# Optimization experiments

Measured on AMD Instinct MI355X. Metric: run time of the kernel, lower is better.

## Reference

```python
import jax, jax.numpy as jnp
import numpy as np
import math

B, SEQ, E, H, NB, NHYP = 4, 1024, 512, 8, 64, 6
V, HID, NC, ENC = 32000, 2048, 6, 6
DH = E // H


def _pos_encoding(n, e, dtype):
    pos = jnp.arange(n, dtype=dtype)[:, None]
    div = jnp.exp(-jnp.arange(0, e, 2, dtype=dtype) * (math.log(10000.0) / e))
    ang = pos * div  # [n, e/2]
    pe = jnp.zeros((n, e), dtype)
    pe = pe.at[:, 0::2].set(jnp.sin(ang))
    pe = pe.at[:, 1::2].set(jnp.cos(ang))
    return pe


def _layer_norm(x, g, b):
    m = x.mean(-1, keepdims=True)
    v = ((x - m) ** 2).mean(-1, keepdims=True)
    return (x - m) / jnp.sqrt(v + 1e-5) * g + b


def _lsh_attention(x, Wq, bq, Wv, bv, hyper):
    b, n, e = x.shape
    q = x @ Wq + bq
    v = x @ Wv + bv
    q4 = q.reshape(b, n, H, DH)  # [b,n,h,d]
    v4 = v.reshape(b, n, H, DH)
    # bucket hashing: append bias 1, project on hyperplanes, binarize, binary-encode
    aug = jnp.concatenate([q4, jnp.ones((b, n, H, 1), q.dtype)], axis=-1)
    proj = jnp.einsum('bnhe,ey->bnhy', aug, hyper)
    bits = (proj >= 0).astype(q.dtype)
    pows = (2 ** jnp.arange(NHYP)).astype(q.dtype)
    buckets = jnp.einsum('bnhy,y->bnh', bits, pows).astype(jnp.int32)
    bh = buckets.transpose(0, 2, 1)  # [b,h,n]
    qh = q4.transpose(0, 2, 1, 3)  # [b,h,n,d]
    vh = v4.transpose(0, 2, 1, 3)
    scores = jnp.einsum('bhnd,bhmd->bhnm', qh, qh) / math.sqrt(e)
    # torch code zeroes q rows at their OWN bucket and sums q_c @ q_c^T over all
    # NB buckets; that equals scores * (NB - 2 + [bucket_i == bucket_j]) exactly.
    same = bh[:, :, :, None] == bh[:, :, None, :]
    count = (NB - 2 + same.astype(jnp.int32)).astype(scores.dtype)
    attn = jax.nn.softmax(scores * count, axis=-1)
    out = jnp.einsum('bhnm,bhmd->bhnd', attn, vh)
    return out.transpose(0, 2, 1, 3).reshape(b, n, e)


def setup_inputs() -> dict:
    key = jax.random.key(0)
    ks = jax.random.split(key, 16)
    s = 0.02
    emb = jax.random.normal(ks[0], (V, E), jnp.float32) * s
    emb = emb.at[V - 1].set(0.0)  # padding_idx row
    return dict(
        inputs=jax.random.randint(ks[1], (B, SEQ), 0, V),
        emb=emb,
        gamma=jnp.ones((E,), jnp.float32),
        beta=jnp.zeros((E,), jnp.float32),
        Wq=jax.random.normal(ks[2], (E, E), jnp.float32) * s,
        bq=jnp.zeros((E,), jnp.float32),
        Wv=jax.random.normal(ks[3], (E, E), jnp.float32) * s,
        bv=jnp.zeros((E,), jnp.float32),
        hyper=jax.random.normal(ks[4], (DH + 1, NHYP), jnp.float32),
        W1=jax.random.normal(ks[5], (E, HID), jnp.float32) * s,
        b1=jnp.zeros((HID,), jnp.float32),
        W2=jax.random.normal(ks[6], (HID, E), jnp.float32) * s,
        b2=jnp.zeros((E,), jnp.float32),
        Wm=jax.random.normal(ks[7], (E * SEQ, NC), jnp.float32) * 0.002,
        bm=jnp.zeros((NC,), jnp.float32),
    )


def reference(inputs, emb, gamma, beta, Wq, bq, Wv, bv, hyper, W1, b1, W2, b2, Wm, bm):
    x = emb[inputs]  # [B, SEQ, E]
    x = x + _pos_encoding(x.shape[1], x.shape[2], x.dtype)
    for _ in range(ENC):  # shared weights across encoders
        a = _lsh_attention(x, Wq, bq, Wv, bv, hyper)
        x = _layer_norm(a, gamma, beta)
        x = jax.nn.relu(x @ W1 + b1) @ W2 + b2 + x
        x = _layer_norm(x, gamma, beta)
    x = x.reshape(x.shape[0], -1)
    return x @ Wm + bm  # [B, NC]
```

## Files before the change

kernel.cpp:

```cpp
#include <hip/hip_runtime.h>
#include <hip/hip_bf16.h>
#include <math.h>

#define B_    4
#define SEQ_  1024
#define E_    512
#define H_    8
#define DH_   64
#define NHYP_ 6
#define HID_  2048
#define NC_   6
#define ENC_  6
#define BH_   (B_*H_)
#define NCAT_ 1088

typedef __attribute__((ext_vector_type(8))) short short8;
typedef __attribute__((ext_vector_type(4))) float f32x4;

static __device__ __forceinline__ float wave_rsum(float v){
#pragma unroll
  for(int o=32;o;o>>=1) v += __shfl_down(v,o,64);
  return v;
}
static __device__ __forceinline__ ushort f2b(float v){
  __hip_bfloat16 h = __float2bfloat16(v);
  return *(ushort*)&h;
}
static __device__ __forceinline__ float b2f(ushort u){
  unsigned int x = ((unsigned int)u) << 16;
  return *(float*)&x;
}
static __device__ __forceinline__ void gload16(const void* g, void* l){
  __builtin_amdgcn_global_load_lds(
      (const __attribute__((address_space(1))) void*)g,
      (__attribute__((address_space(3))) void*)l,
      16, 0, 0);
}

__global__ void embed_pe_kernel(const int* __restrict__ inp, const float* __restrict__ emb,
                                float* __restrict__ x, ushort* __restrict__ xh){
  int row = blockIdx.x;
  int s = row & (SEQ_-1);
  int idx = inp[row];
  const float* er = emb + (size_t)idx*E_;
  float* xr = x + (size_t)row*E_;
  ushort* hr = xh + (size_t)row*E_;
  for(int c=threadIdx.x;c<E_;c+=blockDim.x){
    int i = c>>1;
    float div = expf(-(float)i * 0.0359778920780319646f);
    float ang = (float)s * div;
    float pe = (c&1) ? cosf(ang) : sinf(ang);
    float v = er[c] + pe;
    xr[c] = v;
    hr[c] = f2b(v);
  }
}

__global__ __launch_bounds__(256) void transpose_cast(
    const float* __restrict__ W, ushort* __restrict__ Wt, int K, int N){
  __shared__ float T[32][33];
  int tx = threadIdx.x & 31, ty = threadIdx.x >> 5;
  int n0 = blockIdx.x*32, k0 = blockIdx.y*32;
#pragma unroll
  for(int i=0;i<32;i+=8) T[ty+i][tx] = W[(size_t)(k0+ty+i)*N + n0+tx];
  __syncthreads();
#pragma unroll
  for(int i=0;i<32;i+=8)
    Wt[(size_t)(n0+ty+i)*K + k0+tx] = f2b(T[tx][ty+i]);
}

__global__ void wproj_build(const float* __restrict__ Wq, const float* __restrict__ hyper,
                            ushort* __restrict__ WcatT){
  int t = blockIdx.x*256 + threadIdx.x;
  int c = t >> 9, k = t & 511;
  float s = 0.f;
  if(c < 48){
    int h = c/6, y = c%6;
    const float* wr = Wq + (size_t)k*E_ + h*DH_;
    for(int d=0;d<DH_;++d) s += wr[d]*hyper[d*NHYP_+y];
  }
  WcatT[(size_t)(1024+c)*E_ + k] = f2b(s);
}

__global__ void bias_build(const float* __restrict__ bq, const float* __restrict__ bv,
                           const float* __restrict__ hyper, float* __restrict__ bcat){
  int t = blockIdx.x*256 + threadIdx.x;
  if(t >= NCAT_) return;
  float v;
  if(t < 512) v = bq[t];
  else if(t < 1024) v = bv[t-512];
  else if(t < 1072){
    int c = t - 1024, h = c/6, y = c%6;
    float s = hyper[DH_*NHYP_ + y];
    for(int d=0;d<DH_;++d) s += bq[h*DH_+d]*hyper[d*NHYP_+y];
    v = s;
  } else v = 0.f;
  bcat[t] = v;
}

template<int BM, int BN, int EPI>
__global__ __launch_bounds__(256) void gemm_mfma(
    const ushort* __restrict__ A, const ushort* __restrict__ Bt,
    const float* __restrict__ bias, const float* __restrict__ res,
    void* __restrict__ C0, void* __restrict__ C1, void* __restrict__ C2,
    int M, int N, int K)
{
  constexpr int MI = BM/32, NI = BN/32;
  constexpr int ACH = BM/32, BCH = BN/32;
  __shared__ ushort As[2][BM*64];
  __shared__ ushort Bs[2][BN*64];
  int tid = threadIdx.x;
  int w = tid>>6, lane = tid&63, g = lane>>4, li = lane&15;
  int wr = w>>1, wc = w&1;
  int bm = blockIdx.y*BM, bn = blockIdx.x*BN;
  int NK = K>>6;

  f32x4 acc[MI][NI] = {};

  auto issue = [&](int ks, int pb){
    int k0 = ks*64;
#pragma unroll
    for(int it=0; it<ACH; ++it){
      int c = it*256 + tid; int r = c>>3; int kq = ((c&7)^(r&7))*8;
      gload16(&A[(size_t)(bm+r)*K + k0 + kq], &As[pb][it*2048 + w*512]);
    }
#pragma unroll
    for(int it=0; it<BCH; ++it){
      int c = it*256 + tid; int r = c>>3; int kq = ((c&7)^(r&7))*8;
      gload16(&Bt[(size_t)(bn+r)*K + k0 + kq], &Bs[pb][it*2048 + w*512]);
    }
  };

  issue(0, 0);
  __syncthreads();
  for(int ks=0; ks<NK; ++ks){
    if(ks+1 < NK) issue(ks+1, (ks+1)&1);
    int pb = ks&1;
#pragma unroll
    for(int kc=0; kc<2; ++kc){
      short8 af[MI], bf[NI];
#pragma unroll
      for(int mi=0;mi<MI;++mi)
        af[mi] = *(const short8*)&As[pb][(wr*(BM/2)+mi*16+li)*64 + (((kc*4+g)^(li&7))*8)];
#pragma unroll
      for(int ni=0;ni<NI;++ni)
        bf[ni] = *(const short8*)&Bs[pb][(wc*(BN/2)+ni*16+li)*64 + (((kc*4+g)^(li&7))*8)];
#pragma unroll
      for(int mi=0;mi<MI;++mi)
#pragma unroll
        for(int ni=0;ni<NI;++ni)
          acc[mi][ni] = __builtin_amdgcn_mfma_f32_16x16x32_bf16(af[mi], bf[ni], acc[mi][ni], 0,0,0);
    }
    __syncthreads();
  }

#pragma unroll
  for(int mi=0;mi<MI;++mi){
    int rbase = bm + wr*(BM/2) + mi*16 + g*4;
#pragma unroll
    for(int ni=0;ni<NI;++ni){
      int cc = bn + wc*(BN/2) + ni*16 + li;
      float bv = bias[cc];
      float vv[4];
#pragma unroll
      for(int j=0;j<4;++j) vv[j] = acc[mi][ni][j] + bv;
      if(EPI==0){
#pragma unroll
        for(int j=0;j<4;++j) ((float*)C0)[(size_t)(rbase+j)*N + cc] = vv[j];
      } else if(EPI==1){
#pragma unroll
        for(int j=0;j<4;++j) ((ushort*)C0)[(size_t)(rbase+j)*N + cc] = f2b(fmaxf(vv[j],0.0f));
      } else if(EPI==2){
#pragma unroll
        for(int j=0;j<4;++j){
          size_t o = (size_t)(rbase+j)*N + cc;
          ((float*)C0)[o] = vv[j] + res[o];
        }
      } else {
        if(cc < 512){
          int h = cc>>6, d = cc&63;
#pragma unroll
          for(int j=0;j<4;++j){
            int r = rbase + j;
            int b = r>>10, n = r&1023;
            ((ushort*)C1)[(((size_t)(b*8+h))*1024 + n)*64 + d] = f2b(vv[j]);
          }
        } else if(cc < 1024){
          int cl = cc - 512; int h = cl>>6, d = cl&63;
          int b = rbase>>10, n = rbase&1023;
          ushort4 pk;
          pk.x = f2b(vv[0]); pk.y = f2b(vv[1]); pk.z = f2b(vv[2]); pk.w = f2b(vv[3]);
          *(ushort4*)&((ushort*)C2)[(((size_t)(b*8+h))*64 + d)*1024 + n] = pk;
        } else if(cc < 1072){
#pragma unroll
          for(int j=0;j<4;++j)
            ((float*)C0)[(size_t)(rbase+j)*64 + (cc-1024)] = vv[j];
        }
      }
    }
  }
}

__global__ __launch_bounds__(256) void encode_kernel(
    const ushort* __restrict__ Qh, const float* __restrict__ Pr,
    int* __restrict__ buckets, float* __restrict__ qn2){
  int t = blockIdx.x*256 + threadIdx.x;
  int h = t & 7, row = t >> 3;
  int b = row >> 10, n = row & 1023;
  int bhn = (b*8+h)*1024 + n;
  const short8* qp = (const short8*)&Qh[(size_t)bhn*DH_];
  float s2 = 0.f;
#pragma unroll
  for(int c=0;c<8;++c){
    short8 v = qp[c];
#pragma unroll
    for(int j=0;j<8;++j){
      float f = b2f((ushort)v[j]);
      s2 += f*f;
    }
  }
  qn2[bhn] = s2;
  const float* pr = Pr + (size_t)row*64 + h*NHYP_;
  int bk = 0;
#pragma unroll
  for(int y=0;y<NHYP_;++y) bk |= (pr[y] >= 0.0f) ? (1<<y) : 0;
  buckets[bhn] = bk;
}

__global__ __launch_bounds__(256) void attn_mfma_kernel(
    const ushort* __restrict__ Qh,
    const ushort* __restrict__ Vt,
    const int* __restrict__ buckets,
    const float* __restrict__ qn2,
    float* __restrict__ outp)
{
  int bid = blockIdx.x;
  int bh = bid & 31;
  int qt = bid >> 5;
  int b = bh >> 3, h = bh & 7;
  int tid = threadIdx.x;
  int w = tid >> 6, lane = tid & 63;
  int g = lane >> 4, li = lane & 15;

  __shared__ ushort Ks[2][64*64];
  __shared__ ushort Vs[2][64*64];
  __shared__ ushort Ps[64*68];
  __shared__ int bks[2][64];
  __shared__ int bqs[64];
  __shared__ float mred[4];

  const ushort* Qbase = Qh + (size_t)bh*SEQ_*DH_;
  const ushort* Vbase = Vt + (size_t)bh*DH_*SEQ_;
  const int* Bb = buckets + bh*SEQ_;
  const float* qn = qn2 + bh*SEQ_;
  int q0 = qt*64;

  auto issue = [&](int kt, int pb){
    int j0 = kt*64;
#pragma unroll
    for(int it=0; it<2; ++it){
      int c = it*256 + tid; int r = c>>3; int ks = ((c&7)^(r&7))*8;
      gload16(&Qbase[(size_t)(j0+r)*DH_ + ks], &Ks[pb][it*2048 + w*512]);
      gload16(&Vbase[(size_t)r*SEQ_ + j0 + ks], &Vs[pb][it*2048 + w*512]);
    }
    if(tid < 16) gload16(&Bb[j0 + tid*4], &bks[pb][0]);
  };

  issue(0, 0);
  short8 qa[2];
  int qrow = q0 + w*16 + li;
#pragma unroll
  for(int kc=0; kc<2; ++kc)
    qa[kc] = *(const short8*)&Qbase[(size_t)qrow*DH_ + kc*32 + g*8];
  if(tid < 64) bqs[tid] = Bb[q0 + tid];

  float mx = 0.f;
  for(int i=tid;i<SEQ_;i+=256) mx = fmaxf(mx, qn[i]);
#pragma unroll
  for(int o=32;o;o>>=1) mx = fmaxf(mx, __shfl_xor(mx, o, 64));
  if(lane==0) mred[w] = mx;
  __syncthreads();
  float maxn = sqrtf(fmaxf(fmaxf(mred[0],mred[1]), fmaxf(mred[2],mred[3])));

  const float invsq = 0.04419417382415922f;
  const float c63 = invsq * 63.0f;
  float Mrow[4];
#pragma unroll
  for(int i=0;i<4;++i)
    Mrow[i] = c63 * sqrtf(qn[q0 + w*16 + g*4 + i]) * maxn + 1.0f;

  f32x4 acc_o[4] = {};
  float psum[4] = {0.f,0.f,0.f,0.f};

  for(int kt=0; kt<16; ++kt){
    if(kt < 15) issue(kt+1, (kt+1)&1);
    int pb = kt&1;

    f32x4 accs[4];
    __builtin_amdgcn_s_setprio(1);
#pragma unroll
    for(int nt=0; nt<4; ++nt){
      f32x4 z = {};
#pragma unroll
      for(int kc=0; kc<2; ++kc){
        short8 kb = *(const short8*)&Ks[pb][(nt*16+li)*64 + (((kc*4+g)^(li&7))*8)];
        z = __builtin_amdgcn_mfma_f32_16x16x32_bf16(qa[kc], kb, z, 0,0,0);
      }
      accs[nt] = z;
    }
    __builtin_amdgcn_s_setprio(0);
    int bkc[4];
#pragma unroll
    for(int nt=0;nt<4;++nt) bkc[nt] = bks[pb][nt*16 + li];

#pragma unroll
    for(int i=0;i<4;++i){
      int rloc = w*16 + g*4 + i;
      int bq = bqs[rloc];
      float rs = 0.f;
#pragma unroll
      for(int nt=0;nt<4;++nt){
        float cnt = (bkc[nt] == bq) ? 63.f : 62.f;
        float e = __expf(accs[nt][i] * (invsq * cnt) - Mrow[i]);
        rs += e;
        Ps[rloc*68 + nt*16 + li] = f2b(e);
      }
      psum[i] += rs;
    }
    __builtin_amdgcn_s_setprio(1);
#pragma unroll
    for(int dt=0; dt<4; ++dt){
      f32x4 z = acc_o[dt];
#pragma unroll
      for(int kc=0; kc<2; ++kc){
        short8 pa = *(const short8*)&Ps[(w*16+li)*68 + kc*32 + g*8];
        short8 vb = *(const short8*)&Vs[pb][(dt*16+li)*64 + (((kc*4+g)^(li&7))*8)];
        z = __builtin_amdgcn_mfma_f32_16x16x32_bf16(pa, vb, z, 0,0,0);
      }
      acc_o[dt] = z;
    }
    __builtin_amdgcn_s_setprio(0);
    __syncthreads();
  }
#pragma unroll
  for(int i=0;i<4;++i){
#pragma unroll
    for(int o=8;o;o>>=1) psum[i] += __shfl_xor(psum[i], o, 64);
  }
  float* obase = outp + ((size_t)(b*SEQ_ + q0 + w*16 + g*4))*E_ + h*DH_;
#pragma unroll
  for(int i=0;i<4;++i){
    float inv = 1.0f / fmaxf(psum[i], 1e-35f);
#pragma unroll
    for(int dt=0;dt<4;++dt)
      obase[(size_t)i*E_ + dt*16 + li] = acc_o[dt][i] * inv;
  }
}

__global__ __launch_bounds__(256) void ln_kernel(
    const float* __restrict__ in, const float* __restrict__ g,
    const float* __restrict__ bb, float* __restrict__ outp,
    ushort* __restrict__ oh){
  int row = blockIdx.x*4 + (threadIdx.x>>6);
  int lane = threadIdx.x & 63;
  const float4* xr = (const float4*)(in + (size_t)row*E_);
  float4 v0 = xr[lane*2], v1 = xr[lane*2+1];
  float s  = v0.x+v0.y+v0.z+v0.w + v1.x+v1.y+v1.z+v1.w;
  float s2 = v0.x*v0.x+v0.y*v0.y+v0.z*v0.z+v0.w*v0.w
           + v1.x*v1.x+v1.y*v1.y+v1.z*v1.z+v1.w*v1.w;
#pragma unroll
  for(int o=32;o;o>>=1){ s += __shfl_xor(s,o,64); s2 += __shfl_xor(s2,o,64); }
  float mean = s*(1.0f/E_);
  float var  = s2*(1.0f/E_) - mean*mean;
  float inv = rsqrtf(var + 1e-5f);
  const float4* g4 = (const float4*)(g) + lane*2;
  const float4* b4 = (const float4*)(bb) + lane*2;
  float4 g0 = g4[0], g1 = g4[1], b0 = b4[0], b1 = b4[1];
  float4 y0, y1;
  y0.x=(v0.x-mean)*inv*g0.x+b0.x; y0.y=(v0.y-mean)*inv*g0.y+b0.y;
  y0.z=(v0.z-mean)*inv*g0.z+b0.z; y0.w=(v0.w-mean)*inv*g0.w+b0.w;
  y1.x=(v1.x-mean)*inv*g1.x+b1.x; y1.y=(v1.y-mean)*inv*g1.y+b1.y;
  y1.z=(v1.z-mean)*inv*g1.z+b1.z; y1.w=(v1.w-mean)*inv*g1.w+b1.w;
  float4* orow = (float4*)(outp + (size_t)row*E_) + lane*2;
  orow[0] = y0; orow[1] = y1;
  ushort hs[8];
  hs[0]=f2b(y0.x); hs[1]=f2b(y0.y); hs[2]=f2b(y0.z); hs[3]=f2b(y0.w);
  hs[4]=f2b(y1.x); hs[5]=f2b(y1.y); hs[6]=f2b(y1.z); hs[7]=f2b(y1.w);
  *(uint4*)&oh[(size_t)row*E_ + lane*8] = *(uint4*)hs;
}

__global__ void final_partial(const float* __restrict__ x, const float* __restrict__ Wm,
                              float* __restrict__ part){
  int b  = blockIdx.x >> 7;
  int ch = blockIdx.x & 127;
  const float* xb = x + (size_t)b*SEQ_*E_;
  int k0 = ch*4096;
  float acc[NC_] = {};
  for(int k=k0+threadIdx.x; k<k0+4096; k+=256){
    float xv = xb[k];
    const float* wrow = Wm + (size_t)k*NC_;
#pragma unroll
    for(int c=0;c<NC_;++c) acc[c] += xv*wrow[c];
  }
#pragma unroll
  for(int c=0;c<NC_;++c) acc[c] = wave_rsum(acc[c]);
  __shared__ float r[4][NC_];
  int w = threadIdx.x>>6, lane = threadIdx.x&63;
  if(lane==0){
#pragma unroll
    for(int c=0;c<NC_;++c) r[w][c] = acc[c];
  }
  __syncthreads();
  if(threadIdx.x==0){
#pragma unroll
    for(int c=0;c<NC_;++c)
      part[(size_t)blockIdx.x*NC_ + c] = r[0][c]+r[1][c]+r[2][c]+r[3][c];
  }
}

__global__ void final_reduce(const float* __restrict__ part, const float* __restrict__ bm,
                             float* __restrict__ out){
  int t = threadIdx.x;
  if(t >= B_*NC_) return;
  int b = t / NC_, c = t % NC_;
  float s = bm[c];
  for(int i=0;i<128;++i) s += part[(size_t)(b*128+i)*NC_ + c];
  out[t] = s;
}

extern "C" void kernel_launch(void* const* d_in, const int* in_sizes, int n_in,
                              void* d_out, int out_size, void* d_ws, size_t ws_size,
                              hipStream_t stream){
  const int*   inp   = (const int*)d_in[0];
  const float* emb   = (const float*)d_in[1];
  const float* gamma = (const float*)d_in[2];
  const float* beta  = (const float*)d_in[3];
  const float* Wq    = (const float*)d_in[4];
  const float* bq    = (const float*)d_in[5];
  const float* Wv    = (const float*)d_in[6];
  const float* bv    = (const float*)d_in[7];
  const float* hyper = (const float*)d_in[8];
  const float* W1    = (const float*)d_in[9];
  const float* b1    = (const float*)d_in[10];
  const float* W2    = (const float*)d_in[11];
  const float* b2    = (const float*)d_in[12];
  const float* Wm    = (const float*)d_in[13];
  const float* bm    = (const float*)d_in[14];
  float* out = (float*)d_out;

  char* ws = (char*)d_ws;
  size_t off = 0;
  auto alloc = [&](size_t bytes)->void*{
    void* p = ws + off; off += (bytes + 255) & ~(size_t)255; return p;
  };
  const size_t NTOK = (size_t)B_*SEQ_;
  float*  X    = (float*)alloc(NTOK*E_*sizeof(float));
  float*  A    = (float*)alloc(NTOK*E_*sizeof(float));
  float*  Pr   = (float*)alloc(NTOK*64*sizeof(float));
  ushort* Xh   = (ushort*)alloc(NTOK*E_*sizeof(ushort));
  ushort* Hh   = (ushort*)alloc(NTOK*HID_*sizeof(ushort));
  int*    Bk   = (int*)  alloc((size_t)BH_*SEQ_*sizeof(int));
  float*  Qn2  = (float*)alloc((size_t)BH_*SEQ_*sizeof(float));
  float*  Pp   = (float*)alloc((size_t)B_*128*NC_*sizeof(float));
  ushort* Qh   = (ushort*)alloc((size_t)BH_*SEQ_*DH_*sizeof(ushort));
  ushort* Vt   = (ushort*)alloc((size_t)BH_*DH_*SEQ_*sizeof(ushort));
  ushort* WcatT= (ushort*)alloc((size_t)NCAT_*E_*sizeof(ushort));
  ushort* W1T  = (ushort*)alloc((size_t)HID_*E_*sizeof(ushort));
  ushort* W2T  = (ushort*)alloc((size_t)E_*HID_*sizeof(ushort));
  float*  bcat = (float*)alloc(NCAT_*sizeof(float));
  (void)ws_size; (void)in_sizes; (void)n_in; (void)out_size;

  transpose_cast<<<dim3(E_/32,  E_/32),  256, 0, stream>>>(Wq, WcatT, E_, E_);
  transpose_cast<<<dim3(E_/32,  E_/32),  256, 0, stream>>>(Wv, WcatT + (size_t)512*E_, E_, E_);
  wproj_build<<<128, 256, 0, stream>>>(Wq, hyper, WcatT);
  transpose_cast<<<dim3(HID_/32,E_/32),  256, 0, stream>>>(W1, W1T, E_, HID_);
  transpose_cast<<<dim3(E_/32,  HID_/32),256, 0, stream>>>(W2, W2T, HID_, E_);
  bias_build<<<5, 256, 0, stream>>>(bq, bv, hyper, bcat);

  embed_pe_kernel<<<B_*SEQ_, 256, 0, stream>>>(inp, emb, X, Xh);

  dim3 gQV(NCAT_/64, (B_*SEQ_)/128);
  dim3 gF1(HID_/128, (B_*SEQ_)/128);
  dim3 gF2(E_/64,    (B_*SEQ_)/128);
  for(int l=0;l<ENC_;++l){
    gemm_mfma<128,64,5><<<gQV, 256, 0, stream>>>(Xh, WcatT, bcat, nullptr, Pr, Qh, Vt, B_*SEQ_, NCAT_, E_);
    encode_kernel<<<(B_*SEQ_*H_)/256, 256, 0, stream>>>(Qh, Pr, Bk, Qn2);
    attn_mfma_kernel<<<BH_*16, 256, 0, stream>>>(Qh, Vt, Bk, Qn2, A);
    ln_kernel<<<B_*SEQ_/4, 256, 0, stream>>>(A, gamma, beta, X, Xh);
    gemm_mfma<128,128,1><<<gF1, 256, 0, stream>>>(Xh, W1T, b1, nullptr, Hh, nullptr, nullptr, B_*SEQ_, HID_, E_);
    gemm_mfma<128,64,2><<<gF2, 256, 0, stream>>>(Hh, W2T, b2, X, A, nullptr, nullptr, B_*SEQ_, E_, HID_);
    ln_kernel<<<B_*SEQ_/4, 256, 0, stream>>>(A, gamma, beta, X, Xh);
  }
  final_partial<<<B_*128, 256, 0, stream>>>(X, Wm, Pp);
  final_reduce<<<1, 32, 0, stream>>>(Pp, bm, out);
}
```

Measured before the change: 650.5 us.

## Split attention keys across two blocks and fuse partial combine into layernorm

Attention now splits the key range into two halves, each handled by a separate block. Each block writes unnormalized partial outputs and row sums, and a new combine_ln kernel adds the halves, normalizes and applies layernorm. This doubles the attention grid from 512 to 1024 blocks to fill the GPU's CUs better, and the QV and FF2 GEMMs move to 64-row tiles for more blocks. It works because the softmax uses a fixed per-row bound rather than a running max, so the halves can be summed directly. The cost is extra partial-output traffic (two fp32 copies of the attention output) plus a per-block duplicated max-norm scan.

```diff
diff --git a/kernel.cpp b/kernel.cpp
--- a/kernel.cpp
+++ b/kernel.cpp
@@ -12,6 +12,7 @@
 #define NC_   6
 #define ENC_  6
 #define BH_   (B_*H_)
+#define NTOK_ 4096
 #define NCAT_ 1088
 
 typedef __attribute__((ext_vector_type(8))) short short8;
@@ -232,11 +233,13 @@
     const ushort* __restrict__ Vt,
     const int* __restrict__ buckets,
     const float* __restrict__ qn2,
-    float* __restrict__ outp)
+    float* __restrict__ Op,
+    float* __restrict__ Sp)
 {
   int bid = blockIdx.x;
-  int bh = bid & 31;
-  int qt = bid >> 5;
+  int bh   = bid & 31;
+  int half = (bid >> 5) & 1;
+  int qt   = bid >> 6;
   int b = bh >> 3, h = bh & 7;
   int tid = threadIdx.x;
   int w = tid >> 6, lane = tid & 63;
@@ -254,6 +257,7 @@
   const int* Bb = buckets + bh*SEQ_;
   const float* qn = qn2 + bh*SEQ_;
   int q0 = qt*64;
+  int kt0 = half*8;
 
   auto issue = [&](int kt, int pb){
     int j0 = kt*64;
@@ -266,7 +270,7 @@
     if(tid < 16) gload16(&Bb[j0 + tid*4], &bks[pb][0]);
   };
 
-  issue(0, 0);
+  issue(kt0, 0);
   short8 qa[2];
   int qrow = q0 + w*16 + li;
 #pragma unroll
@@ -292,9 +296,10 @@
   f32x4 acc_o[4] = {};
   float psum[4] = {0.f,0.f,0.f,0.f};
 
-  for(int kt=0; kt<16; ++kt){
-    if(kt < 15) issue(kt+1, (kt+1)&1);
-    int pb = kt&1;
+  for(int t=0; t<8; ++t){
+    int kt = kt0 + t;
+    if(t < 7) issue(kt+1, (t+1)&1);
+    int pb = t&1;
 
     f32x4 accs[4];
     __builtin_amdgcn_s_setprio(1);
@@ -347,14 +352,59 @@
 #pragma unroll
     for(int o=8;o;o>>=1) psum[i] += __shfl_xor(psum[i], o, 64);
   }
-  float* obase = outp + ((size_t)(b*SEQ_ + q0 + w*16 + g*4))*E_ + h*DH_;
+  float* obase = Op + (size_t)half*NTOK_*E_
+               + ((size_t)(b*SEQ_ + q0 + w*16 + g*4))*E_ + h*DH_;
 #pragma unroll
   for(int i=0;i<4;++i){
-    float inv = 1.0f / fmaxf(psum[i], 1e-35f);
 #pragma unroll
     for(int dt=0;dt<4;++dt)
-      obase[(size_t)i*E_ + dt*16 + li] = acc_o[dt][i] * inv;
-  }
+      obase[(size_t)i*E_ + dt*16 + li] = acc_o[dt][i];
+  }
+  if(li == 0){
+    float* sp = Sp + (size_t)half*BH_*SEQ_ + (size_t)bh*SEQ_ + q0 + w*16 + g*4;
+#pragma unroll
+    for(int i=0;i<4;++i) sp[i] = psum[i];
+  }
+}
+
+__global__ __launch_bounds__(256) void combine_ln(
+    const float* __restrict__ Op, const float* __restrict__ Sp,
+    const float* __restrict__ g, const float* __restrict__ bb,
+    float* __restrict__ outp, ushort* __restrict__ oh){
+  int row = blockIdx.x*4 + (threadIdx.x>>6);
+  int lane = threadIdx.x & 63;
+  int b = row >> 10, n = row & 1023;
+  int h = lane >> 3;
+  size_t sidx = (size_t)(b*8+h)*SEQ_ + n;
+  float ps = Sp[sidx] + Sp[(size_t)BH_*SEQ_ + sidx];
+  float inv0 = 1.0f / fmaxf(ps, 1e-35f);
+  const float4* o1 = (const float4*)(Op + (size_t)row*E_) + lane*2;
+  const float4* o2 = (const float4*)(Op + (size_t)NTOK_*E_ + (size_t)row*E_) + lane*2;
+  float4 v0 = o1[0], v1 = o1[1], u0 = o2[0], u1 = o2[1];
+  v0.x=(v0.x+u0.x)*inv0; v0.y=(v0.y+u0.y)*inv0; v0.z=(v0.z+u0.z)*inv0; v0.w=(v0.w+u0.w)*inv0;
+  v1.x=(v1.x+u1.x)*inv0; v1.y=(v1.y+u1.y)*inv0; v1.z=(v1.z+u1.z)*inv0; v1.w=(v1.w+u1.w)*inv0;
+  float s  = v0.x+v0.y+v0.z+v0.w + v1.x+v1.y+v1.z+v1.w;
+  float s2 = v0.x*v0.x+v0.y*v0.y+v0.z*v0.z+v0.w*v0.w
+           + v1.x*v1.x+v1.y*v1.y+v1.z*v1.z+v1.w*v1.w;
+#pragma unroll
+  for(int o=32;o;o>>=1){ s += __shfl_xor(s,o,64); s2 += __shfl_xor(s2,o,64); }
+  float mean = s*(1.0f/E_);
+  float var  = s2*(1.0f/E_) - mean*mean;
+  float inv = rsqrtf(var + 1e-5f);
+  const float4* g4 = (const float4*)(g) + lane*2;
+  const float4* b4 = (const float4*)(bb) + lane*2;
+  float4 g0 = g4[0], g1 = g4[1], b0 = b4[0], b1 = b4[1];
+  float4 y0, y1;
+  y0.x=(v0.x-mean)*inv*g0.x+b0.x; y0.y=(v0.y-mean)*inv*g0.y+b0.y;
+  y0.z=(v0.z-mean)*inv*g0.z+b0.z; y0.w=(v0.w-mean)*inv*g0.w+b0.w;
+  y1.x=(v1.x-mean)*inv*g1.x+b1.x; y1.y=(v1.y-mean)*inv*g1.y+b1.y;
+  y1.z=(v1.z-mean)*inv*g1.z+b1.z; y1.w=(v1.w-mean)*inv*g1.w+b1.w;
+  float4* orow = (float4*)(outp + (size_t)row*E_) + lane*2;
+  orow[0] = y0; orow[1] = y1;
+  ushort hs[8];
+  hs[0]=f2b(y0.x); hs[1]=f2b(y0.y); hs[2]=f2b(y0.z); hs[3]=f2b(y0.w);
+  hs[4]=f2b(y1.x); hs[5]=f2b(y1.y); hs[6]=f2b(y1.z); hs[7]=f2b(y1.w);
+  *(uint4*)&oh[(size_t)row*E_ + lane*8] = *(uint4*)hs;
 }
 
 __global__ __launch_bounds__(256) void ln_kernel(
@@ -457,6 +507,8 @@
   float*  X    = (float*)alloc(NTOK*E_*sizeof(float));
   float*  A    = (float*)alloc(NTOK*E_*sizeof(float));
   float*  Pr   = (float*)alloc(NTOK*64*sizeof(float));
+  float*  Op   = (float*)alloc((size_t)2*NTOK*E_*sizeof(float));
+  float*  Sp   = (float*)alloc((size_t)2*BH_*SEQ_*sizeof(float));
   ushort* Xh   = (ushort*)alloc(NTOK*E_*sizeof(ushort));
   ushort* Hh   = (ushort*)alloc(NTOK*HID_*sizeof(ushort));
   int*    Bk   = (int*)  alloc((size_t)BH_*SEQ_*sizeof(int));
@@ -479,16 +531,16 @@
 
   embed_pe_kernel<<<B_*SEQ_, 256, 0, stream>>>(inp, emb, X, Xh);
 
-  dim3 gQV(NCAT_/64, (B_*SEQ_)/128);
+  dim3 gQV(NCAT_/64, (B_*SEQ_)/64);
   dim3 gF1(HID_/128, (B_*SEQ_)/128);
-  dim3 gF2(E_/64,    (B_*SEQ_)/128);
+  dim3 gF2(E_/64,    (B_*SEQ_)/64);
   for(int l=0;l<ENC_;++l){
-    gemm_mfma<128,64,5><<<gQV, 256, 0, stream>>>(Xh, WcatT, bcat, nullptr, Pr, Qh, Vt, B_*SEQ_, NCAT_, E_);
+    gemm_mfma<64,64,5><<<gQV, 256, 0, stream>>>(Xh, WcatT, bcat, nullptr, Pr, Qh, Vt, B_*SEQ_, NCAT_, E_);
     encode_kernel<<<(B_*SEQ_*H_)/256, 256, 0, stream>>>(Qh, Pr, Bk, Qn2);
-    attn_mfma_kernel<<<BH_*16, 256, 0, stream>>>(Qh, Vt, Bk, Qn2, A);
-    ln_kernel<<<B_*SEQ_/4, 256, 0, stream>>>(A, gamma, beta, X, Xh);
+    attn_mfma_kernel<<<BH_*32, 256, 0, stream>>>(Qh, Vt, Bk, Qn2, Op, Sp);
+    combine_ln<<<B_*SEQ_/4, 256, 0, stream>>>(Op, Sp, gamma, beta, X, Xh);
     gemm_mfma<128,128,1><<<gF1, 256, 0, stream>>>(Xh, W1T, b1, nullptr, Hh, nullptr, nullptr, B_*SEQ_, HID_, E_);
-    gemm_mfma<128,64,2><<<gF2, 256, 0, stream>>>(Hh, W2T, b2, X, A, nullptr, nullptr, B_*SEQ_, E_, HID_);
+    gemm_mfma<64,64,2><<<gF2, 256, 0, stream>>>(Hh, W2T, b2, X, A, nullptr, nullptr, B_*SEQ_, E_, HID_);
     ln_kernel<<<B_*SEQ_/4, 256, 0, stream>>>(A, gamma, beta, X, Xh);
   }
   final_partial<<<B_*128, 256, 0, stream>>>(X, Wm, Pp);
```

New measurement: 642.4 us. Within noise of the previous version (-1.2%).

## Fuse bucket encoding into QV GEMM epilogue and split-K the FFN down-projection

Applied to the files above, without the earlier changes.

The QV projection GEMM epilogue now computes the squared query norms and the hash bucket ids directly, with a cross-lane reduction and shared-memory staging, so the separate encode kernel and the fp32 projection buffer go away. Its tile shrinks to 64x64 for more blocks. The W2 GEMM uses a 2-way split-K with 64x64 tiles and writes two partial results. A new ln2 kernel sums the partials, bias and residual before the layer norm. This trades one launch and some traffic for extra partial-buffer reads and writes and added shared memory in every GEMM instantiation.

```diff
diff --git a/kernel.cpp b/kernel.cpp
--- a/kernel.cpp
+++ b/kernel.cpp
@@ -12,6 +12,7 @@
 #define NC_   6
 #define ENC_  6
 #define BH_   (B_*H_)
+#define NTOK_ 4096
 #define NCAT_ 1088
 
 typedef __attribute__((ext_vector_type(8))) short short8;
@@ -103,22 +104,26 @@
     const ushort* __restrict__ A, const ushort* __restrict__ Bt,
     const float* __restrict__ bias, const float* __restrict__ res,
     void* __restrict__ C0, void* __restrict__ C1, void* __restrict__ C2,
-    int M, int N, int K)
+    void* __restrict__ C3, int M, int N, int K)
 {
   constexpr int MI = BM/32, NI = BN/32;
   constexpr int ACH = BM/32, BCH = BN/32;
   __shared__ ushort As[2][BM*64];
   __shared__ ushort Bs[2][BN*64];
+  __shared__ float epi[64*49];
   int tid = threadIdx.x;
   int w = tid>>6, lane = tid&63, g = lane>>4, li = lane&15;
   int wr = w>>1, wc = w&1;
   int bm = blockIdx.y*BM, bn = blockIdx.x*BN;
-  int NK = K>>6;
+  int kz = blockIdx.z;
+  int kcnt = K / (int)gridDim.z;
+  int kbase = kz * kcnt;
+  int NK = kcnt >> 6;
 
   f32x4 acc[MI][NI] = {};
 
   auto issue = [&](int ks, int pb){
-    int k0 = ks*64;
+    int k0 = kbase + ks*64;
 #pragma unroll
     for(int it=0; it<ACH; ++it){
       int c = it*256 + tid; int r = c>>3; int kq = ((c&7)^(r&7))*8;
@@ -154,22 +159,108 @@
     __syncthreads();
   }
 
+  if(EPI==5){
+    if(bn < 512){
+      int h = bn >> 6;
+#pragma unroll
+      for(int mi=0;mi<MI;++mi){
+        int rbase = bm + wr*(BM/2) + mi*16 + g*4;
+        float q2s[4] = {0.f,0.f,0.f,0.f};
+#pragma unroll
+        for(int ni=0;ni<NI;++ni){
+          int cc = bn + wc*(BN/2) + ni*16 + li;
+          float bv = bias[cc];
+          int d = cc & 63;
+#pragma unroll
+          for(int j=0;j<4;++j){
+            float vvf = acc[mi][ni][j] + bv;
+            ushort ub = f2b(vvf);
+            int r = rbase + j; int b = r>>10, n = r&1023;
+            ((ushort*)C1)[(((size_t)(b*8+h))*1024 + n)*64 + d] = ub;
+            float f = b2f(ub);
+            q2s[j] += f*f;
+          }
+        }
+#pragma unroll
+        for(int j=0;j<4;++j){
+#pragma unroll
+          for(int o=8;o;o>>=1) q2s[j] += __shfl_xor(q2s[j], o, 64);
+        }
+        if(li==0){
+#pragma unroll
+          for(int j=0;j<4;++j)
+            epi[(wr*(BM/2)+mi*16+g*4+j)*2 + wc] = q2s[j];
+        }
+      }
+      __syncthreads();
+      if(tid < 64){
+        int r = bm + tid; int b = r>>10, n = r&1023;
+        ((float*)C3)[((size_t)(b*8+h))*1024 + n] = epi[tid*2] + epi[tid*2+1];
+      }
+    } else if(bn < 1024){
+#pragma unroll
+      for(int mi=0;mi<MI;++mi){
+        int rbase = bm + wr*(BM/2) + mi*16 + g*4;
+        int b = rbase>>10, n = rbase&1023;
+#pragma unroll
+        for(int ni=0;ni<NI;++ni){
+          int cc = bn + wc*(BN/2) + ni*16 + li;
+          float bv = bias[cc];
+          int cl = cc - 512; int h = cl>>6, d = cl&63;
+          ushort4 pk;
+          pk.x = f2b(acc[mi][ni][0]+bv); pk.y = f2b(acc[mi][ni][1]+bv);
+          pk.z = f2b(acc[mi][ni][2]+bv); pk.w = f2b(acc[mi][ni][3]+bv);
+          *(ushort4*)&((ushort*)C2)[(((size_t)(b*8+h))*64 + d)*1024 + n] = pk;
+        }
+      }
+    } else {
+#pragma unroll
+      for(int mi=0;mi<MI;++mi){
+        int rloc = wr*(BM/2) + mi*16 + g*4;
+#pragma unroll
+        for(int ni=0;ni<NI;++ni){
+          int c = wc*(BN/2) + ni*16 + li;
+          if(c < 48){
+            float bv = bias[1024 + c];
+#pragma unroll
+            for(int j=0;j<4;++j)
+              epi[(rloc+j)*49 + c] = acc[mi][ni][j] + bv;
+          }
+        }
+      }
+      __syncthreads();
+      if(tid < 64){
+        int r = bm + tid; int b = r>>10, n = r&1023;
+#pragma unroll
+        for(int h=0;h<8;++h){
+          int bk = 0;
+#pragma unroll
+          for(int y=0;y<NHYP_;++y)
+            bk |= (epi[tid*49 + h*NHYP_ + y] >= 0.0f) ? (1<<y) : 0;
+          ((int*)C0)[((size_t)(b*8+h))*1024 + n] = bk;
+        }
+      }
+    }
+    return;
+  }
+
 #pragma unroll
   for(int mi=0;mi<MI;++mi){
     int rbase = bm + wr*(BM/2) + mi*16 + g*4;
 #pragma unroll
     for(int ni=0;ni<NI;++ni){
       int cc = bn + wc*(BN/2) + ni*16 + li;
-      float bv = bias[cc];
+      float bv = (EPI==6) ? 0.0f : bias[cc];
       float vv[4];
 #pragma unroll
       for(int j=0;j<4;++j) vv[j] = acc[mi][ni][j] + bv;
-      if(EPI==0){
-#pragma unroll
-        for(int j=0;j<4;++j) ((float*)C0)[(size_t)(rbase+j)*N + cc] = vv[j];
-      } else if(EPI==1){
+      if(EPI==1){
 #pragma unroll
         for(int j=0;j<4;++j) ((ushort*)C0)[(size_t)(rbase+j)*N + cc] = f2b(fmaxf(vv[j],0.0f));
+      } else if(EPI==6){
+        float* dst = (float*)C0 + (size_t)kz*M*N;
+#pragma unroll
+        for(int j=0;j<4;++j) dst[(size_t)(rbase+j)*N + cc] = vv[j];
       } else if(EPI==2){
 #pragma unroll
         for(int j=0;j<4;++j){
@@ -177,54 +268,11 @@
           ((float*)C0)[o] = vv[j] + res[o];
         }
       } else {
-        if(cc < 512){
-          int h = cc>>6, d = cc&63;
-#pragma unroll
-          for(int j=0;j<4;++j){
-            int r = rbase + j;
-            int b = r>>10, n = r&1023;
-            ((ushort*)C1)[(((size_t)(b*8+h))*1024 + n)*64 + d] = f2b(vv[j]);
-          }
-        } else if(cc < 1024){
-          int cl = cc - 512; int h = cl>>6, d = cl&63;
-          int b = rbase>>10, n = rbase&1023;
-          ushort4 pk;
-          pk.x = f2b(vv[0]); pk.y = f2b(vv[1]); pk.z = f2b(vv[2]); pk.w = f2b(vv[3]);
-          *(ushort4*)&((ushort*)C2)[(((size_t)(b*8+h))*64 + d)*1024 + n] = pk;
-        } else if(cc < 1072){
-#pragma unroll
-          for(int j=0;j<4;++j)
-            ((float*)C0)[(size_t)(rbase+j)*64 + (cc-1024)] = vv[j];
-        }
-      }
-    }
-  }
-}
-
-__global__ __launch_bounds__(256) void encode_kernel(
-    const ushort* __restrict__ Qh, const float* __restrict__ Pr,
-    int* __restrict__ buckets, float* __restrict__ qn2){
-  int t = blockIdx.x*256 + threadIdx.x;
-  int h = t & 7, row = t >> 3;
-  int b = row >> 10, n = row & 1023;
-  int bhn = (b*8+h)*1024 + n;
-  const short8* qp = (const short8*)&Qh[(size_t)bhn*DH_];
-  float s2 = 0.f;
-#pragma unroll
-  for(int c=0;c<8;++c){
-    short8 v = qp[c];
-#pragma unroll
-    for(int j=0;j<8;++j){
-      float f = b2f((ushort)v[j]);
-      s2 += f*f;
-    }
-  }
-  qn2[bhn] = s2;
-  const float* pr = Pr + (size_t)row*64 + h*NHYP_;
-  int bk = 0;
-#pragma unroll
-  for(int y=0;y<NHYP_;++y) bk |= (pr[y] >= 0.0f) ? (1<<y) : 0;
-  buckets[bhn] = bk;
+#pragma unroll
+        for(int j=0;j<4;++j) ((float*)C0)[(size_t)(rbase+j)*N + cc] = vv[j];
+      }
+    }
+  }
 }
 
 __global__ __launch_bounds__(256) void attn_mfma_kernel(
@@ -365,6 +413,47 @@
   int lane = threadIdx.x & 63;
   const float4* xr = (const float4*)(in + (size_t)row*E_);
   float4 v0 = xr[lane*2], v1 = xr[lane*2+1];
+  float s  = v0.x+v0.y+v0.z+v0.w + v1.x+v1.y+v1.z+v1.w;
+  float s2 = v0.x*v0.x+v0.y*v0.y+v0.z*v0.z+v0.w*v0.w
+           + v1.x*v1.x+v1.y*v1.y+v1.z*v1.z+v1.w*v1.w;
+#pragma unroll
+  for(int o=32;o;o>>=1){ s += __shfl_xor(s,o,64); s2 += __shfl_xor(s2,o,64); }
+  float mean = s*(1.0f/E_);
+  float var  = s2*(1.0f/E_) - mean*mean;
+  float inv = rsqrtf(var + 1e-5f);
+  const float4* g4 = (const float4*)(g) + lane*2;
+  const float4* b4 = (const float4*)(bb) + lane*2;
+  float4 g0 = g4[0], g1 = g4[1], b0 = b4[0], b1 = b4[1];
+  float4 y0, y1;
+  y0.x=(v0.x-mean)*inv*g0.x+b0.x; y0.y=(v0.y-mean)*inv*g0.y+b0.y;
+  y0.z=(v0.z-mean)*inv*g0.z+b0.z; y0.w=(v0.w-mean)*inv*g0.w+b0.w;
+  y1.x=(v1.x-mean)*inv*g1.x+b1.x; y1.y=(v1.y-mean)*inv*g1.y+b1.y;
+  y1.z=(v1.z-mean)*inv*g1.z+b1.z; y1.w=(v1.w-mean)*inv*g1.w+b1.w;
+  float4* orow = (float4*)(outp + (size_t)row*E_) + lane*2;
+  orow[0] = y0; orow[1] = y1;
+  ushort hs[8];
+  hs[0]=f2b(y0.x); hs[1]=f2b(y0.y); hs[2]=f2b(y0.z); hs[3]=f2b(y0.w);
+  hs[4]=f2b(y1.x); hs[5]=f2b(y1.y); hs[6]=f2b(y1.z); hs[7]=f2b(y1.w);
+  *(uint4*)&oh[(size_t)row*E_ + lane*8] = *(uint4*)hs;
+}
+
+__global__ __launch_bounds__(256) void ln2_kernel(
+    const float* __restrict__ P, const float* __restrict__ b2,
+    const float* __restrict__ Xres, const float* __restrict__ g,
+    const float* __restrict__ bb, float* __restrict__ outp,
+    ushort* __restrict__ oh){
+  int row = blockIdx.x*4 + (threadIdx.x>>6);
+  int lane = threadIdx.x & 63;
+  const float4* p0 = (const float4*)(P + (size_t)row*E_) + lane*2;
+  const float4* p1 = (const float4*)(P + (size_t)NTOK_*E_ + (size_t)row*E_) + lane*2;
+  const float4* xr = (const float4*)(Xres + (size_t)row*E_) + lane*2;
+  const float4* c4 = (const float4*)(b2) + lane*2;
+  float4 v0 = p0[0], v1 = p0[1], u0 = p1[0], u1 = p1[1];
+  float4 x0 = xr[0], x1 = xr[1], cb0 = c4[0], cb1 = c4[1];
+  v0.x += u0.x + cb0.x + x0.x; v0.y += u0.y + cb0.y + x0.y;
+  v0.z += u0.z + cb0.z + x0.z; v0.w += u0.w + cb0.w + x0.w;
+  v1.x += u1.x + cb1.x + x1.x; v1.y += u1.y + cb1.y + x1.y;
+  v1.z += u1.z + cb1.z + x1.z; v1.w += u1.w + cb1.w + x1.w;
   float s  = v0.x+v0.y+v0.z+v0.w + v1.x+v1.y+v1.z+v1.w;
   float s2 = v0.x*v0.x+v0.y*v0.y+v0.z*v0.z+v0.w*v0.w
            + v1.x*v1.x+v1.y*v1.y+v1.z*v1.z+v1.w*v1.w;
@@ -456,7 +545,7 @@
   const size_t NTOK = (size_t)B_*SEQ_;
   float*  X    = (float*)alloc(NTOK*E_*sizeof(float));
   float*  A    = (float*)alloc(NTOK*E_*sizeof(float));
-  float*  Pr   = (float*)alloc(NTOK*64*sizeof(float));
+  float*  Op   = (float*)alloc((size_t)2*NTOK*E_*sizeof(float));
   ushort* Xh   = (ushort*)alloc(NTOK*E_*sizeof(ushort));
   ushort* Hh   = (ushort*)alloc(NTOK*HID_*sizeof(ushort));
   int*    Bk   = (int*)  alloc((size_t)BH_*SEQ_*sizeof(int));
@@ -479,17 +568,16 @@
 
   embed_pe_kernel<<<B_*SEQ_, 256, 0, stream>>>(inp, emb, X, Xh);
 
-  dim3 gQV(NCAT_/64, (B_*SEQ_)/128);
+  dim3 gQV(NCAT_/64, (B_*SEQ_)/64);
   dim3 gF1(HID_/128, (B_*SEQ_)/128);
-  dim3 gF2(E_/64,    (B_*SEQ_)/128);
+  dim3 gF2(E_/64,    (B_*SEQ_)/64, 2);
   for(int l=0;l<ENC_;++l){
-    gemm_mfma<128,64,5><<<gQV, 256, 0, stream>>>(Xh, WcatT, bcat, nullptr, Pr, Qh, Vt, B_*SEQ_, NCAT_, E_);
-    encode_kernel<<<(B_*SEQ_*H_)/256, 256, 0, stream>>>(Qh, Pr, Bk, Qn2);
+    gemm_mfma<64,64,5><<<gQV, 256, 0, stream>>>(Xh, WcatT, bcat, nullptr, Bk, Qh, Vt, Qn2, B_*SEQ_, NCAT_, E_);
     attn_mfma_kernel<<<BH_*16, 256, 0, stream>>>(Qh, Vt, Bk, Qn2, A);
     ln_kernel<<<B_*SEQ_/4, 256, 0, stream>>>(A, gamma, beta, X, Xh);
-    gemm_mfma<128,128,1><<<gF1, 256, 0, stream>>>(Xh, W1T, b1, nullptr, Hh, nullptr, nullptr, B_*SEQ_, HID_, E_);
-    gemm_mfma<128,64,2><<<gF2, 256, 0, stream>>>(Hh, W2T, b2, X, A, nullptr, nullptr, B_*SEQ_, E_, HID_);
-    ln_kernel<<<B_*SEQ_/4, 256, 0, stream>>>(A, gamma, beta, X, Xh);
+    gemm_mfma<128,128,1><<<gF1, 256, 0, stream>>>(Xh, W1T, b1, nullptr, Hh, nullptr, nullptr, nullptr, B_*SEQ_, HID_, E_);
+    gemm_mfma<64,64,6><<<gF2, 256, 0, stream>>>(Hh, W2T, b2, nullptr, Op, nullptr, nullptr, nullptr, B_*SEQ_, E_, HID_);
+    ln2_kernel<<<B_*SEQ_/4, 256, 0, stream>>>(Op, b2, X, gamma, beta, X, Xh);
   }
   final_partial<<<B_*128, 256, 0, stream>>>(X, Wm, Pp);
   final_reduce<<<1, 32, 0, stream>>>(Pp, bm, out);
```

Result: faster. 588.4 us (-9.5%).
